# Kernel tuning notes

Hardware: AMD Instinct MI355X
Metric: run time of the kernel (lower is better)

## Reference

```python
import jax, jax.numpy as jnp
import numpy as np

B, S, D, H, NU, T = 32, 2048, 512, 4, 10000, 24
HD = D // H
N = B * S


def setup_inputs() -> dict:
    key = jax.random.key(0)
    ks = jax.random.split(key, 19)
    sc = 0.02  # weight init scale for numerical sanity
    return {
        "timeslot_embedded": jax.random.normal(ks[0], (T, D), jnp.float32),
        "smoothed_timeslot_embedded": jax.random.normal(ks[1], (T, D), jnp.float32),
        "user_embedded": jax.random.normal(ks[2], (NU, D), jnp.float32),
        "user_x": jax.random.randint(ks[3], (B,), 0, NU, jnp.int64) if jax.config.jax_enable_x64 else jax.random.randint(ks[3], (B,), 0, NU).astype(jnp.int32),
        "hour_x": jax.random.randint(ks[4], (B, S), 0, T).astype(jnp.int32),
        "hour_mask": jnp.zeros((B, S, T), jnp.int32),
        "user_pref_table": jax.random.normal(ks[5], (NU, D), jnp.float32),
        "Wq": jax.random.normal(ks[6], (H, 2 * D, HD), jnp.float32) * sc,
        "bq": jax.random.normal(ks[7], (H, HD), jnp.float32) * sc,
        "Wk": jax.random.normal(ks[8], (H, D, HD), jnp.float32) * sc,
        "bk": jax.random.normal(ks[9], (H, HD), jnp.float32) * sc,
        "Wv": jax.random.normal(ks[10], (H, D, HD), jnp.float32) * sc,
        "bv": jax.random.normal(ks[11], (H, HD), jnp.float32) * sc,
        "Wu": jax.random.normal(ks[12], (D, D), jnp.float32) * sc,
        "bu": jax.random.normal(ks[13], (D,), jnp.float32) * sc,
        "Wt": jax.random.normal(ks[14], (D, T), jnp.float32) * sc,
        "bt": jax.random.normal(ks[15], (T,), jnp.float32) * sc,
        "osc_u": jax.random.normal(ks[16], (H, N, T), jnp.float32),
        "osc_v": jax.random.normal(ks[17], (H, N, T), jnp.float32),
    }


def reference(timeslot_embedded, smoothed_timeslot_embedded, user_embedded,
              user_x, hour_x, hour_mask, user_pref_table,
              Wq, bq, Wk, bk, Wv, bv, Wu, bu, Wt, bt, osc_u, osc_v):
    b, s = hour_x.shape
    n = b * s
    d = user_pref_table.shape[-1]
    hd = Wq.shape[-1]
    hour_flat = hour_x.reshape(n)
    mask_flat = hour_mask.reshape(n, -1)  # [N, 24]

    # user preference gathered per batch, repeated along sequence
    user_feat = jnp.broadcast_to(user_pref_table[user_x][:, None, :], (b, s, d)).reshape(n, d)
    time_feat = timeslot_embedded[hour_flat]            # [N, D]
    query = jnp.concatenate([user_feat, time_feat], -1)  # [N, 2D]

    q = jnp.einsum('nd,hde->hne', query, Wq) + bq[:, None, :]                     # [H,N,hd]
    k = jnp.einsum('td,hde->hte', smoothed_timeslot_embedded, Wk) + bk[:, None, :]  # [H,24,hd]
    v = jnp.einsum('td,hde->hte', smoothed_timeslot_embedded, Wv) + bv[:, None, :]  # [H,24,hd]

    scale = 1.0 / jnp.sqrt(jnp.float32(hd))
    scores = jnp.einsum('hne,hte->hnt', q, k) * scale  # [H, N, 24]
    scores = jnp.where(mask_flat[None] == 1, -jnp.inf, scores)

    u0 = osc_u * 0.01
    v0 = osc_v * 0.01

    # 50-step chaotic oscillator recurrence (a1=a2=b1=5, b2=-5). NOTE: in the
    # original torch code the loop result is discarded (Calculatez is re-called
    # after the loop, drawing fresh noise); retained here for faithfulness.
    def osc_step(carry, _):
        u, vv = carry
        u = jax.nn.relu(5.0 * u + 5.0 * vv + scores)  # uthreshold = 0
        vv = jax.nn.relu(5.0 * u + 5.0 * vv)          # b1*u - b2*v, b2=-5; vthreshold = 0
        return (u, vv), None

    _dead = jax.lax.scan(osc_step, (u0, v0), None, length=50)[0]

    # final Calculatez: z = (u - v) * exp(k * I^2) + relu(I), k = -500
    z = (u0 - v0) * jnp.exp(-500.0 * scores * scores) + jax.nn.relu(scores)
    attn = jax.nn.softmax(z, axis=-1)                  # [H, N, 24]
    out = jnp.einsum('hnt,hte->hne', attn, v)          # [H, N, hd]
    head_out = jnp.transpose(out, (1, 0, 2)).reshape(n, -1)  # [N, D]

    at_emb = (head_out @ Wu + bu).reshape(b, s, -1)
    time_logits = (head_out @ Wt + bt).reshape(b, s, -1)
    return (at_emb, time_logits)
```

## Files before the change

kernel.cpp:

```cpp
#include <hip/hip_runtime.h>
#include <hip/hip_bf16.h>

typedef __bf16 bf16;
typedef __bf16 bf16x8 __attribute__((ext_vector_type(8)));
typedef float f32x4 __attribute__((ext_vector_type(4)));

#define NB 32
#define SS 2048
#define NN 65536
#define DD 512
#define HH 4
#define HD 128
#define TT 24


__global__ __launch_bounds__(256) void prep1(
    const float* __restrict__ tslot, const float* __restrict__ smooth,
    const int* __restrict__ user_x, const float* __restrict__ upref,
    const float* __restrict__ Wq, const float* __restrict__ bq,
    const float* __restrict__ Wk, const float* __restrict__ bk,
    const float* __restrict__ Wv, const float* __restrict__ bv,
    float* __restrict__ ws_k, float* __restrict__ ws_v,
    float* __restrict__ ws_qt, float* __restrict__ ws_qu)
{
    int gid = blockIdx.x * 256 + threadIdx.x;
    if (gid < 12288) {
        int e = gid & 127; int th = gid >> 7; int t = th % TT; int h = th / TT;
        const float* x = smooth + t * DD;
        const float* w = Wk + (size_t)(h * DD) * HD + e;
        float acc = bk[h * HD + e];
        #pragma unroll 8
        for (int d = 0; d < DD; ++d) acc += x[d] * w[(size_t)d * HD];
        ws_k[gid] = acc;
    } else if (gid < 24576) {
        int idx = gid - 12288;
        int e = idx & 127; int th = idx >> 7; int t = th % TT; int h = th / TT;
        const float* x = smooth + t * DD;
        const float* w = Wv + (size_t)(h * DD) * HD + e;
        float acc = bv[h * HD + e];
        #pragma unroll 8
        for (int d = 0; d < DD; ++d) acc += x[d] * w[(size_t)d * HD];
        ws_v[idx] = acc;
    } else if (gid < 36864) {
        int idx = gid - 24576;
        int e = idx & 127; int th = idx >> 7; int t = th % TT; int h = th / TT;
        const float* x = tslot + t * DD;
        const float* w = Wq + (size_t)(h * 2 * DD + DD) * HD + e;
        float acc = bq[h * HD + e];
        #pragma unroll 8
        for (int d = 0; d < DD; ++d) acc += x[d] * w[(size_t)d * HD];
        ws_qt[idx] = acc;
    } else {
        int idx = gid - 36864;
        int e = idx & 127; int b = (idx >> 7) & 31; int h = idx >> 12;
        const float* x = upref + (size_t)user_x[b] * DD;
        const float* w = Wq + (size_t)(h * 2 * DD) * HD + e;
        float acc = 0.f;
        #pragma unroll 8
        for (int d = 0; d < DD; ++d) acc += x[d] * w[(size_t)d * HD];
        ws_qu[idx] = acc;
    }
}

__global__ __launch_bounds__(256) void prep2(
    const float* __restrict__ ws_k, const float* __restrict__ ws_v,
    const float* __restrict__ ws_qt, const float* __restrict__ ws_qu,
    const float* __restrict__ Wu, const float* __restrict__ bu,
    const float* __restrict__ Wt, const float* __restrict__ bt,
    float* __restrict__ ws_su, float* __restrict__ ws_st,
    float* __restrict__ ws_b2, bf16* __restrict__ ws_w2t)
{
    int gid = blockIdx.x * 256 + threadIdx.x;
    if (gid < 3072) {
        int tp = gid % TT; int hb = gid / TT;
        const float* q = ws_qu + hb * HD;
        int h = hb >> 5;
        const float* kk = ws_k + (h * TT + tp) * HD;
        float acc = 0.f;
        #pragma unroll 8
        for (int e = 0; e < HD; ++e) acc += q[e] * kk[e];
        ws_su[gid] = acc;
    } else if (gid < 5376) {
        int idx = gid - 3072;
        int tp = idx % TT; int ht = idx / TT; int h = ht / TT;
        const float* q = ws_qt + ht * HD;
        const float* kk = ws_k + (h * TT + tp) * HD;
        float acc = 0.f;
        #pragma unroll 8
        for (int e = 0; e < HD; ++e) acc += q[e] * kk[e];
        ws_st[idx] = acc;
    } else if (gid < 5376 + 52224) {
        int idx = gid - 5376;
        int i = idx % 96; int j = idx / 96;
        int h = i / TT;
        const float* vv = ws_v + i * HD;
        float acc = 0.f;
        if (j < 512) {
            const float* w = Wu + (size_t)(h * HD) * DD + j;
            #pragma unroll 8
            for (int e = 0; e < HD; ++e) acc += vv[e] * w[(size_t)e * DD];
        } else if (j < 536) {
            const float* w = Wt + (size_t)(h * HD) * TT + (j - 512);
            #pragma unroll 8
            for (int e = 0; e < HD; ++e) acc += vv[e] * w[(size_t)e * TT];
        }
        ws_w2t[j * 96 + i] = (bf16)acc;
    } else if (gid < 5376 + 52224 + 544) {
        int j = gid - (5376 + 52224);
        float val = (j < 512) ? bu[j] : ((j < 536) ? bt[j - 512] : 0.f);
        ws_b2[j] = val;
    }
}

__global__ __launch_bounds__(256) void fused_main(
    const int* __restrict__ hour_x, const int* __restrict__ hour_mask,
    const float* __restrict__ osc_u, const float* __restrict__ osc_v,
    const float* __restrict__ ws_su, const float* __restrict__ ws_st,
    const float* __restrict__ ws_b2, const bf16* __restrict__ ws_w2t,
    float* __restrict__ out_at, float* __restrict__ out_tl)
{
    __shared__ bf16 attn_lds[64][104];

    const int tid = threadIdx.x;
    const int h = tid >> 6;
    const int r = tid & 63;
    const int n0 = blockIdx.x * 64;
    const int n = n0 + r;
    const int b = n >> 11;
    const int hour = hour_x[n];

    const float* su = ws_su + (h * NB + b) * TT;
    const float* st = ws_st + (h * TT + hour) * TT;
    const int*   mk = hour_mask + (size_t)n * TT;
    const float* up = osc_u + (size_t)(h * NN + n) * TT;
    const float* vp = osc_v + (size_t)(h * NN + n) * TT;

    float ub[24], vb[24], sub[24], stb[24];
    int mb[24];
    #pragma unroll
    for (int i = 0; i < 6; ++i) {
        *(float4*)(ub + i * 4)  = *(const float4*)(up + i * 4);
        *(float4*)(vb + i * 4)  = *(const float4*)(vp + i * 4);
        *(int4*)(mb + i * 4)    = *(const int4*)(mk + i * 4);
        *(float4*)(sub + i * 4) = *(const float4*)(su + i * 4);
        *(float4*)(stb + i * 4) = *(const float4*)(st + i * 4);
    }

    float z[24];
    float mx = -3.4e38f;
    #pragma unroll
    for (int t = 0; t < 24; ++t) {
        float s = (sub[t] + stb[t]) * 0.08838834764831845f;
        float du = 0.01f * ub[t] - 0.01f * vb[t];
        float g = __expf(-500.0f * s * s);
        float zz = du * g + fmaxf(s, 0.0f);
        zz = (mb[t] == 1) ? 0.0f : zz;
        z[t] = zz;
        mx = fmaxf(mx, zz);
    }
    float ssum = 0.f;
    #pragma unroll
    for (int t = 0; t < 24; ++t) { float p = __expf(z[t] - mx); z[t] = p; ssum += p; }
    float inv = 1.0f / ssum;
    #pragma unroll
    for (int t = 0; t < 24; ++t) attn_lds[r][h * TT + t] = (bf16)(z[t] * inv);

    __syncthreads();

    const int w    = tid >> 6;
    const int lane = tid & 63;
    const int m16  = lane & 15;
    const int quad = lane >> 4;

    for (int ct = w; ct < 34; ct += 4) {
        const int c0 = ct * 16;
        const int c  = c0 + m16;
        bf16x8 bfr[3];
        #pragma unroll
        for (int kk = 0; kk < 3; ++kk)
            bfr[kk] = *(const bf16x8*)(ws_w2t + c * 96 + kk * 32 + quad * 8);
        const float bias = ws_b2[c];

        #pragma unroll
        for (int rt = 0; rt < 4; ++rt) {
            f32x4 acc = {0.f, 0.f, 0.f, 0.f};
            #pragma unroll
            for (int kk = 0; kk < 3; ++kk) {
                bf16x8 afr = *(const bf16x8*)(&attn_lds[rt * 16 + m16][kk * 32 + quad * 8]);
                acc = __builtin_amdgcn_mfma_f32_16x16x32_bf16(afr, bfr[kk], acc, 0, 0, 0);
            }
            #pragma unroll
            for (int reg = 0; reg < 4; ++reg) {
                const int gr = n0 + rt * 16 + quad * 4 + reg;
                const float val = acc[reg] + bias;
                if (c < 512)      out_at[(size_t)gr * DD + c] = val;
                else if (c < 536) out_tl[(size_t)gr * TT + (c - 512)] = val;
            }
        }
    }
}

extern "C" void kernel_launch(void* const* d_in, const int* in_sizes, int n_in,
                              void* d_out, int out_size, void* d_ws, size_t ws_size,
                              hipStream_t stream)
{
    const float* tslot  = (const float*)d_in[0];
    const float* smooth = (const float*)d_in[1];
    const int*  user_x = (const int*)d_in[3];
    const int*  hour_x = (const int*)d_in[4];
    const int*  hour_mask = (const int*)d_in[5];
    const float* upref  = (const float*)d_in[6];
    const float* Wq = (const float*)d_in[7];
    const float* bq = (const float*)d_in[8];
    const float* Wk = (const float*)d_in[9];
    const float* bk = (const float*)d_in[10];
    const float* Wv = (const float*)d_in[11];
    const float* bv = (const float*)d_in[12];
    const float* Wu = (const float*)d_in[13];
    const float* bu = (const float*)d_in[14];
    const float* Wt = (const float*)d_in[15];
    const float* bt = (const float*)d_in[16];
    const float* osc_u = (const float*)d_in[17];
    const float* osc_v = (const float*)d_in[18];

    char* ws = (char*)d_ws;
    float* ws_su = (float*)(ws + 0);
    float* ws_st = (float*)(ws + 12288);
    float* ws_b2 = (float*)(ws + 21504);
    float* ws_k  = (float*)(ws + 23680);
    float* ws_v  = (float*)(ws + 72832);
    float* ws_qt = (float*)(ws + 121984);
    float* ws_qu = (float*)(ws + 171136);
    bf16*  ws_w2t = (bf16*)(ws + 236672);

    float* out_at = (float*)d_out;
    float* out_tl = out_at + (size_t)NN * DD;

    prep1<<<208, 256, 0, stream>>>(tslot, smooth, user_x, upref, Wq, bq, Wk, bk,
                                   Wv, bv, ws_k, ws_v, ws_qt, ws_qu);
    prep2<<<228, 256, 0, stream>>>(ws_k, ws_v, ws_qt, ws_qu, Wu, bu, Wt, bt,
                                   ws_su, ws_st, ws_b2, ws_w2t);
    fused_main<<<NN / 64, 256, 0, stream>>>(hour_x, hour_mask, osc_u, osc_v,
                                            ws_su, ws_st, ws_b2, ws_w2t,
                                            out_at, out_tl);
}
```

Measured before the change: 301.1 us.

## Swap MFMA operands for vectorized nontemporal output stores and split prep accumulators

The main kernel swaps the MFMA A/B operands so each lane holds four consecutive output columns of one row. The output and bias are then written as 16-byte nontemporal vector stores instead of scalar strided stores, and the attention row is packed into bf16x8 vectors for LDS writes. The prep1 dot products also use four independent accumulators to break the serial FMA chain. Risks include alignment assumptions on the vector stores into the 24-wide time_logits rows, and changed floating-point summation order.

```diff
diff --git a/kernel.cpp b/kernel.cpp
--- a/kernel.cpp
+++ b/kernel.cpp
@@ -24,42 +24,45 @@
     float* __restrict__ ws_qt, float* __restrict__ ws_qu)
 {
     int gid = blockIdx.x * 256 + threadIdx.x;
+    const float* x; const float* w; float acc;
+    float* dst;
     if (gid < 12288) {
         int e = gid & 127; int th = gid >> 7; int t = th % TT; int h = th / TT;
-        const float* x = smooth + t * DD;
-        const float* w = Wk + (size_t)(h * DD) * HD + e;
-        float acc = bk[h * HD + e];
-        #pragma unroll 8
-        for (int d = 0; d < DD; ++d) acc += x[d] * w[(size_t)d * HD];
-        ws_k[gid] = acc;
+        x = smooth + t * DD;
+        w = Wk + (size_t)(h * DD) * HD + e;
+        acc = bk[h * HD + e];
+        dst = ws_k + gid;
     } else if (gid < 24576) {
         int idx = gid - 12288;
         int e = idx & 127; int th = idx >> 7; int t = th % TT; int h = th / TT;
-        const float* x = smooth + t * DD;
-        const float* w = Wv + (size_t)(h * DD) * HD + e;
-        float acc = bv[h * HD + e];
-        #pragma unroll 8
-        for (int d = 0; d < DD; ++d) acc += x[d] * w[(size_t)d * HD];
-        ws_v[idx] = acc;
+        x = smooth + t * DD;
+        w = Wv + (size_t)(h * DD) * HD + e;
+        acc = bv[h * HD + e];
+        dst = ws_v + idx;
     } else if (gid < 36864) {
         int idx = gid - 24576;
         int e = idx & 127; int th = idx >> 7; int t = th % TT; int h = th / TT;
-        const float* x = tslot + t * DD;
-        const float* w = Wq + (size_t)(h * 2 * DD + DD) * HD + e;
-        float acc = bq[h * HD + e];
-        #pragma unroll 8
-        for (int d = 0; d < DD; ++d) acc += x[d] * w[(size_t)d * HD];
-        ws_qt[idx] = acc;
+        x = tslot + t * DD;
+        w = Wq + (size_t)(h * 2 * DD + DD) * HD + e;
+        acc = bq[h * HD + e];
+        dst = ws_qt + idx;
     } else {
         int idx = gid - 36864;
         int e = idx & 127; int b = (idx >> 7) & 31; int h = idx >> 12;
-        const float* x = upref + (size_t)user_x[b] * DD;
-        const float* w = Wq + (size_t)(h * 2 * DD) * HD + e;
-        float acc = 0.f;
-        #pragma unroll 8
-        for (int d = 0; d < DD; ++d) acc += x[d] * w[(size_t)d * HD];
-        ws_qu[idx] = acc;
-    }
+        x = upref + (size_t)user_x[b] * DD;
+        w = Wq + (size_t)(h * 2 * DD) * HD + e;
+        acc = 0.f;
+        dst = ws_qu + idx;
+    }
+    float a0 = 0.f, a1 = 0.f, a2 = 0.f, a3 = 0.f;
+    #pragma unroll 4
+    for (int d = 0; d < 128; ++d) {
+        a0 += x[d]       * w[(size_t)(d)       * HD];
+        a1 += x[d + 128] * w[(size_t)(d + 128) * HD];
+        a2 += x[d + 256] * w[(size_t)(d + 256) * HD];
+        a3 += x[d + 384] * w[(size_t)(d + 384) * HD];
+    }
+    *dst = acc + ((a0 + a1) + (a2 + a3));
 }
 
 __global__ __launch_bounds__(256) void prep2(
@@ -162,8 +165,15 @@
     #pragma unroll
     for (int t = 0; t < 24; ++t) { float p = __expf(z[t] - mx); z[t] = p; ssum += p; }
     float inv = 1.0f / ssum;
-    #pragma unroll
-    for (int t = 0; t < 24; ++t) attn_lds[r][h * TT + t] = (bf16)(z[t] * inv);
+
+    bf16x8 pk[3];
+    #pragma unroll
+    for (int i = 0; i < 3; ++i)
+        #pragma unroll
+        for (int j = 0; j < 8; ++j) pk[i][j] = (bf16)(z[i * 8 + j] * inv);
+    #pragma unroll
+    for (int i = 0; i < 3; ++i)
+        *(bf16x8*)(&attn_lds[r][h * TT + i * 8]) = pk[i];
 
     __syncthreads();
 
@@ -174,27 +184,28 @@
 
     for (int ct = w; ct < 34; ct += 4) {
         const int c0 = ct * 16;
-        const int c  = c0 + m16;
-        bf16x8 bfr[3];
+        const int cA = c0 + m16;
+        bf16x8 afr[3];
         #pragma unroll
         for (int kk = 0; kk < 3; ++kk)
-            bfr[kk] = *(const bf16x8*)(ws_w2t + c * 96 + kk * 32 + quad * 8);
-        const float bias = ws_b2[c];
+            afr[kk] = *(const bf16x8*)(ws_w2t + cA * 96 + kk * 32 + quad * 8);
+        const int cc0 = c0 + quad * 4;
+        f32x4 bias4 = *(const f32x4*)(ws_b2 + cc0);
 
         #pragma unroll
         for (int rt = 0; rt < 4; ++rt) {
             f32x4 acc = {0.f, 0.f, 0.f, 0.f};
             #pragma unroll
             for (int kk = 0; kk < 3; ++kk) {
-                bf16x8 afr = *(const bf16x8*)(&attn_lds[rt * 16 + m16][kk * 32 + quad * 8]);
-                acc = __builtin_amdgcn_mfma_f32_16x16x32_bf16(afr, bfr[kk], acc, 0, 0, 0);
+                bf16x8 bfr = *(const bf16x8*)(&attn_lds[rt * 16 + m16][kk * 32 + quad * 8]);
+                acc = __builtin_amdgcn_mfma_f32_16x16x32_bf16(afr[kk], bfr, acc, 0, 0, 0);
             }
-            #pragma unroll
-            for (int reg = 0; reg < 4; ++reg) {
-                const int gr = n0 + rt * 16 + quad * 4 + reg;
-                const float val = acc[reg] + bias;
-                if (c < 512)      out_at[(size_t)gr * DD + c] = val;
-                else if (c < 536) out_tl[(size_t)gr * TT + (c - 512)] = val;
+            const int row = n0 + rt * 16 + m16;
+            f32x4 outv = acc + bias4;
+            if (cc0 < 512) {
+                __builtin_nontemporal_store(outv, (f32x4*)(out_at + (size_t)row * DD + cc0));
+            } else if (cc0 < 536) {
+                __builtin_nontemporal_store(outv, (f32x4*)(out_tl + (size_t)row * TT + (cc0 - 512)));
             }
         }
     }
```

Measured after the change: 294.9 us. 2.0% less time.
